# Optimization experiments

Hardware: AMD Instinct MI355X
Metric: run time of the kernel (lower is better)

## Reference

```python
import jax, jax.numpy as jnp
import numpy as np

B, N, C, H, NUM, K = 4, 4096, 256, 512, 4, 10
GS1 = H // NUM   # feature-group size = 128
GS2 = N // NUM   # point-group size  = 1024


def _mlp2(x, w1, b1, w2, b2):
    # Linear -> ReLU -> Linear
    return jax.nn.relu(x @ w1 + b1) @ w2 + b2


def setup_inputs() -> dict:
    key = jax.random.key(0)
    ks = jax.random.split(key, 32)
    s = 0.02
    def w(i, shape):
        return jax.random.normal(ks[i], shape, dtype=jnp.float32) * s
    return {
        "features": jax.random.normal(ks[0], (B, C, N), dtype=jnp.float32),
        "xyz": jax.random.uniform(ks[1], (B, N, 3), dtype=jnp.float32),
        # fc1 / fc2 (stored [in,out] for x @ W)
        "fc1_w": w(2, (C, H)), "fc1_b": jnp.zeros((H,), jnp.float32),
        "fc2_w": w(3, (H, C)), "fc2_b": jnp.zeros((C,), jnp.float32),
        # fc_delta: Linear(3,H) -> ReLU -> Linear(H,H)
        "fd1_w": w(4, (3, H)), "fd1_b": jnp.zeros((H,), jnp.float32),
        "fd2_w": w(5, (H, H)), "fd2_b": jnp.zeros((H,), jnp.float32),
        # fc_gamma: Linear(H,H) -> ReLU -> Linear(H,H)
        "fg1_w": w(6, (H, H)), "fg1_b": jnp.zeros((H,), jnp.float32),
        "fg2_w": w(7, (H, H)), "fg2_b": jnp.zeros((H,), jnp.float32),
        # fc_gamma_2: Linear(GS1,GS1) -> ReLU -> Linear(GS1,GS1)
        "fgh1_w": w(8, (GS1, GS1)), "fgh1_b": jnp.zeros((GS1,), jnp.float32),
        "fgh2_w": w(9, (GS1, GS1)), "fgh2_b": jnp.zeros((GS1,), jnp.float32),
        # projections (no bias)
        "wqs": w(10, (H, H)), "wks": w(11, (H, H)), "wvs": w(12, (H, H)),
        "wqs2": w(13, (GS1, GS1)), "wks2": w(14, (GS1, GS1)),
    }


def reference(features, xyz, fc1_w, fc1_b, fc2_w, fc2_b, fd1_w, fd1_b, fd2_w, fd2_b,
              fg1_w, fg1_b, fg2_w, fg2_b, fgh1_w, fgh1_b, fgh2_w, fgh2_b,
              wqs, wks, wvs, wqs2, wks2):
    pre = features                                  # [B, C, N]
    x = jnp.swapaxes(features, 1, 2) @ fc1_w + fc1_b  # [B, N, H]

    # ---- attn1: feature-group subtraction attention (shared small weights per group)
    xg = x.reshape(B, N, NUM, GS1)
    q1 = jnp.einsum('bngc,cd->bngd', xg, wqs2)
    k1 = jnp.einsum('bngc,cd->bngd', xg, wks2)
    a1 = _mlp2(q1 - k1, fgh1_w, fgh1_b, fgh2_w, fgh2_b)
    a1 = jax.nn.softmax(a1 / np.sqrt(GS1).astype(np.float32), axis=1)  # softmax over points
    attn1 = a1.reshape(B, N, H)

    # ---- attn2: point-group attention. NOTE: source loop reuses stale index `i`
    # (== NUM-1) so every group is computed from the LAST point group; we replicate that.
    gf2 = x[:, (NUM - 1) * GS2:NUM * GS2, :]        # [B, GS2, H]
    q2 = gf2 @ wqs
    k2 = gf2 @ wks
    a2 = _mlp2(q2 - k2, fg1_w, fg1_b, fg2_w, fg2_b)
    a2 = jax.nn.softmax(a2 / np.sqrt(H).astype(np.float32), axis=-2)
    attn2 = jnp.tile(a2, (1, NUM, 1))               # [B, N, H]

    attn = attn1 + attn2
    v = x @ wvs                                     # [B, N, H]

    # ---- KNN positional encoding
    # square_distance
    d = (jnp.sum(xyz ** 2, -1)[:, :, None] + jnp.sum(xyz ** 2, -1)[:, None, :]
         - 2.0 * jnp.einsum('bnd,bmd->bnm', xyz, xyz))  # [B, N, N]
    knn_idx = jax.lax.top_k(-d, K)[1]               # [B, N, K] smallest distances
    knn_xyz = jax.vmap(lambda pts, idx: pts[idx])(xyz, knn_idx)  # [B, N, K, 3]
    pos_enc = _mlp2(xyz[:, :, None, :] - knn_xyz, fd1_w, fd1_b, fd2_w, fd2_b)  # [B,N,K,H]
    pos_enc = pos_enc.mean(axis=2)                  # [B, N, H]

    res = attn * (v + pos_enc)                      # einsum('bmf,bmf->bmf')
    new_features = jnp.swapaxes(res @ fc2_w + fc2_b, 1, 2) + pre  # [B, C, N]
    return (new_features, xyz)
```

## Files before the change

kernel.cpp:

```cpp
#include <hip/hip_runtime.h>
#include <cstdio>

typedef long long ll;
typedef unsigned long long ull;
typedef unsigned short ushort_t;
typedef __bf16 bf16x8 __attribute__((ext_vector_type(8)));
typedef float f32x4 __attribute__((ext_vector_type(4)));
typedef float f32x2 __attribute__((ext_vector_type(2)));

#define BB 4
#define NN 4096
#define CC 256
#define HH 512
#define GNUM 4
#define GS1 128
#define KNN 10

#define SC1 0.08838834764831845f
#define SC2 0.044194173824159216f

__device__ inline unsigned pk2(float x, float y) {
  unsigned a = __float_as_uint(x), b = __float_as_uint(y);
  a = (a + 0x7FFFu + ((a >> 16) & 1u)) >> 16;
  b = (b + 0x7FFFu + ((b >> 16) & 1u)) >> 16;
  return a | (b << 16);
}
__device__ inline ushort_t bf1(float x) {
  unsigned a = __float_as_uint(x);
  return (ushort_t)((a + 0x7FFFu + ((a >> 16) & 1u)) >> 16);
}
__device__ inline float b2f(ushort_t u) { return __uint_as_float((unsigned)u << 16); }
__device__ inline int sw16(int r) { return ((r ^ (r >> 3)) & 7) << 4; }

__device__ inline void xcd_map(int& bx, int& by, int& bz) {
  const int nx = gridDim.x, ny = gridDim.y;
  const int nwg = nx * ny * gridDim.z;
  const int bidf = blockIdx.x + nx * (blockIdx.y + ny * blockIdx.z);
  const int lid = (bidf & 7) * (nwg >> 3) + (bidf >> 3);
  bx = lid % nx;
  const int rem = lid / nx;
  by = rem % ny;
  bz = rem / ny;
}

template<bool ATRANS, bool ABF, bool BSUB, int EPI>
__global__ __launch_bounds__(256, 2) void mgemm_k(
    const void* __restrict__ Ain, const float* __restrict__ Bw,
    const float* __restrict__ Bw2,
    const float* __restrict__ bias, void* __restrict__ CoutV,
    const float* __restrict__ pre,
    int M, int N, int K, int lda, ll strideA, ll strideC)
{
  int bx, by, z;
  xcd_map(bx, by, z);
  const int bm = by * 128;
  const int bn = bx * 128;
  __shared__ alignas(16) char smem[32768];
  char* smA = smem;
  char* smB = smem + 16384;
  const int tid = threadIdx.x;
  const int lane = tid & 63, w = tid >> 6;
  const int lr = lane & 15, lg = lane >> 4;
  const int wm = (w & 1) * 64, wn = (w >> 1) * 64;

  const ushort_t* Ab = ABF ? ((const ushort_t*)Ain + (ll)z * strideA) : nullptr;
  const float*    Af = ABF ? nullptr : ((const float*)Ain + (ll)z * strideA);

  f32x4 acc[4][4] = {};

  for (int k0 = 0; k0 < K; k0 += 64) {
    if (ABF) {
      #pragma unroll
      for (int p = 0; p < 4; ++p) {
        const int i = p * 256 + tid;
        const int r = i >> 3, c8 = (i & 7) * 8;
        const uint4 v = *reinterpret_cast<const uint4*>(Ab + (ll)(bm + r) * lda + (k0 + c8));
        *reinterpret_cast<uint4*>(smA + r * 128 + ((c8 * 2) ^ sw16(r))) = v;
      }
    } else if (ATRANS) {
      #pragma unroll
      for (int p = 0; p < 2; ++p) {
        const int bb = p * 256 + tid;
        const int mb = (bb & 31) * 4, kb = (bb >> 5) * 4;
        const float4 l0 = *reinterpret_cast<const float4*>(Af + (ll)(k0 + kb + 0) * lda + (bm + mb));
        const float4 l1 = *reinterpret_cast<const float4*>(Af + (ll)(k0 + kb + 1) * lda + (bm + mb));
        const float4 l2 = *reinterpret_cast<const float4*>(Af + (ll)(k0 + kb + 2) * lda + (bm + mb));
        const float4 l3 = *reinterpret_cast<const float4*>(Af + (ll)(k0 + kb + 3) * lda + (bm + mb));
        *reinterpret_cast<uint2*>(smA + (mb + 0) * 128 + ((kb * 2) ^ sw16(mb + 0))) = make_uint2(pk2(l0.x, l1.x), pk2(l2.x, l3.x));
        *reinterpret_cast<uint2*>(smA + (mb + 1) * 128 + ((kb * 2) ^ sw16(mb + 1))) = make_uint2(pk2(l0.y, l1.y), pk2(l2.y, l3.y));
        *reinterpret_cast<uint2*>(smA + (mb + 2) * 128 + ((kb * 2) ^ sw16(mb + 2))) = make_uint2(pk2(l0.z, l1.z), pk2(l2.z, l3.z));
        *reinterpret_cast<uint2*>(smA + (mb + 3) * 128 + ((kb * 2) ^ sw16(mb + 3))) = make_uint2(pk2(l0.w, l1.w), pk2(l2.w, l3.w));
      }
    }
    #pragma unroll
    for (int p = 0; p < 2; ++p) {
      const int bb = p * 256 + tid;
      const int nb = (bb & 31) * 4, kb = (bb >> 5) * 4;
      float4 l0 = *reinterpret_cast<const float4*>(Bw + (ll)(k0 + kb + 0) * N + (bn + nb));
      float4 l1 = *reinterpret_cast<const float4*>(Bw + (ll)(k0 + kb + 1) * N + (bn + nb));
      float4 l2 = *reinterpret_cast<const float4*>(Bw + (ll)(k0 + kb + 2) * N + (bn + nb));
      float4 l3 = *reinterpret_cast<const float4*>(Bw + (ll)(k0 + kb + 3) * N + (bn + nb));
      if (BSUB) {
        const float4 m0 = *reinterpret_cast<const float4*>(Bw2 + (ll)(k0 + kb + 0) * N + (bn + nb));
        const float4 m1 = *reinterpret_cast<const float4*>(Bw2 + (ll)(k0 + kb + 1) * N + (bn + nb));
        const float4 m2 = *reinterpret_cast<const float4*>(Bw2 + (ll)(k0 + kb + 2) * N + (bn + nb));
        const float4 m3 = *reinterpret_cast<const float4*>(Bw2 + (ll)(k0 + kb + 3) * N + (bn + nb));
        l0.x -= m0.x; l0.y -= m0.y; l0.z -= m0.z; l0.w -= m0.w;
        l1.x -= m1.x; l1.y -= m1.y; l1.z -= m1.z; l1.w -= m1.w;
        l2.x -= m2.x; l2.y -= m2.y; l2.z -= m2.z; l2.w -= m2.w;
        l3.x -= m3.x; l3.y -= m3.y; l3.z -= m3.z; l3.w -= m3.w;
      }
      *reinterpret_cast<uint2*>(smB + (nb + 0) * 128 + ((kb * 2) ^ sw16(nb + 0))) = make_uint2(pk2(l0.x, l1.x), pk2(l2.x, l3.x));
      *reinterpret_cast<uint2*>(smB + (nb + 1) * 128 + ((kb * 2) ^ sw16(nb + 1))) = make_uint2(pk2(l0.y, l1.y), pk2(l2.y, l3.y));
      *reinterpret_cast<uint2*>(smB + (nb + 2) * 128 + ((kb * 2) ^ sw16(nb + 2))) = make_uint2(pk2(l0.z, l1.z), pk2(l2.z, l3.z));
      *reinterpret_cast<uint2*>(smB + (nb + 3) * 128 + ((kb * 2) ^ sw16(nb + 3))) = make_uint2(pk2(l0.w, l1.w), pk2(l2.w, l3.w));
    }
    __syncthreads();

    #pragma unroll
    for (int ks = 0; ks < 2; ++ks) {
      bf16x8 af[4], bfr[4];
      #pragma unroll
      for (int mi = 0; mi < 4; ++mi) {
        const int r = wm + mi * 16 + lr;
        af[mi] = *reinterpret_cast<const bf16x8*>(smA + r * 128 + ((((ks << 2) + lg) << 4) ^ sw16(r)));
      }
      #pragma unroll
      for (int ni = 0; ni < 4; ++ni) {
        const int r = wn + ni * 16 + lr;
        bfr[ni] = *reinterpret_cast<const bf16x8*>(smB + r * 128 + ((((ks << 2) + lg) << 4) ^ sw16(r)));
      }
      #pragma unroll
      for (int mi = 0; mi < 4; ++mi)
        #pragma unroll
        for (int ni = 0; ni < 4; ++ni)
          acc[mi][ni] = __builtin_amdgcn_mfma_f32_16x16x32_bf16(af[mi], bfr[ni], acc[mi][ni], 0, 0, 0);
    }
    __syncthreads();
  }

  #pragma unroll
  for (int ni = 0; ni < 4; ++ni) {
    const int col = bn + wn + ni * 16 + lr;
    const float bv = (EPI != 0) ? bias[col] : 0.f;
    #pragma unroll
    for (int mi = 0; mi < 4; ++mi) {
      const int row0 = bm + wm + mi * 16 + lg * 4;
      if (EPI == 4) {
        float* Cout = (float*)CoutV;
        const size_t o = ((size_t)z * N + col) * (size_t)M + row0;
        const float4 pv = *reinterpret_cast<const float4*>(pre + o);
        float4 r;
        r.x = acc[mi][ni][0] + bv + pv.x;
        r.y = acc[mi][ni][1] + bv + pv.y;
        r.z = acc[mi][ni][2] + bv + pv.z;
        r.w = acc[mi][ni][3] + bv + pv.w;
        *reinterpret_cast<float4*>(Cout + o) = r;
      } else {
        ushort_t* Co = (ushort_t*)CoutV + (ll)z * strideC;
        #pragma unroll
        for (int i = 0; i < 4; ++i) {
          float val = acc[mi][ni][i] + bv;
          if (EPI == 2) val = fmaxf(val, 0.f);
          Co[(ll)(row0 + i) * N + col] = bf1(val);
        }
      }
    }
  }
}

__global__ __launch_bounds__(256, 2) void gemm_vpe_k(
    const ushort_t* __restrict__ X, const ushort_t* __restrict__ HM,
    const float* __restrict__ wv, const float* __restrict__ w2,
    const float* __restrict__ bias, ushort_t* __restrict__ Cout)
{
  int bx, by, z;
  xcd_map(bx, by, z);
  const int bm = by * 128;
  const int bn = bx * 128;
  __shared__ alignas(16) char smem[32768];
  char* smA = smem;
  char* smB = smem + 16384;
  const int tid = threadIdx.x;
  const int lane = tid & 63, w = tid >> 6;
  const int lr = lane & 15, lg = lane >> 4;
  const int wm = (w & 1) * 64, wn = (w >> 1) * 64;

  f32x4 acc[4][4] = {};

  for (int k0 = 0; k0 < 1024; k0 += 64) {
    const ushort_t* A = (k0 < 512) ? X : HM;
    const float* Bw = (k0 < 512) ? wv : w2;
    const int kk = k0 & 511;
    #pragma unroll
    for (int p = 0; p < 4; ++p) {
      const int i = p * 256 + tid;
      const int r = i >> 3, c8 = (i & 7) * 8;
      const uint4 v = *reinterpret_cast<const uint4*>(A + (ll)(bm + r) * 512 + (kk + c8));
      *reinterpret_cast<uint4*>(smA + r * 128 + ((c8 * 2) ^ sw16(r))) = v;
    }
    #pragma unroll
    for (int p = 0; p < 2; ++p) {
      const int bb = p * 256 + tid;
      const int nb = (bb & 31) * 4, kb = (bb >> 5) * 4;
      const float4 l0 = *reinterpret_cast<const float4*>(Bw + (ll)(kk + kb + 0) * 512 + (bn + nb));
      const float4 l1 = *reinterpret_cast<const float4*>(Bw + (ll)(kk + kb + 1) * 512 + (bn + nb));
      const float4 l2 = *reinterpret_cast<const float4*>(Bw + (ll)(kk + kb + 2) * 512 + (bn + nb));
      const float4 l3 = *reinterpret_cast<const float4*>(Bw + (ll)(kk + kb + 3) * 512 + (bn + nb));
      *reinterpret_cast<uint2*>(smB + (nb + 0) * 128 + ((kb * 2) ^ sw16(nb + 0))) = make_uint2(pk2(l0.x, l1.x), pk2(l2.x, l3.x));
      *reinterpret_cast<uint2*>(smB + (nb + 1) * 128 + ((kb * 2) ^ sw16(nb + 1))) = make_uint2(pk2(l0.y, l1.y), pk2(l2.y, l3.y));
      *reinterpret_cast<uint2*>(smB + (nb + 2) * 128 + ((kb * 2) ^ sw16(nb + 2))) = make_uint2(pk2(l0.z, l1.z), pk2(l2.z, l3.z));
      *reinterpret_cast<uint2*>(smB + (nb + 3) * 128 + ((kb * 2) ^ sw16(nb + 3))) = make_uint2(pk2(l0.w, l1.w), pk2(l2.w, l3.w));
    }
    __syncthreads();

    #pragma unroll
    for (int ks = 0; ks < 2; ++ks) {
      bf16x8 af[4], bfr[4];
      #pragma unroll
      for (int mi = 0; mi < 4; ++mi) {
        const int r = wm + mi * 16 + lr;
        af[mi] = *reinterpret_cast<const bf16x8*>(smA + r * 128 + ((((ks << 2) + lg) << 4) ^ sw16(r)));
      }
      #pragma unroll
      for (int ni = 0; ni < 4; ++ni) {
        const int r = wn + ni * 16 + lr;
        bfr[ni] = *reinterpret_cast<const bf16x8*>(smB + r * 128 + ((((ks << 2) + lg) << 4) ^ sw16(r)));
      }
      #pragma unroll
      for (int mi = 0; mi < 4; ++mi)
        #pragma unroll
        for (int ni = 0; ni < 4; ++ni)
          acc[mi][ni] = __builtin_amdgcn_mfma_f32_16x16x32_bf16(af[mi], bfr[ni], acc[mi][ni], 0, 0, 0);
    }
    __syncthreads();
  }

  #pragma unroll
  for (int ni = 0; ni < 4; ++ni) {
    const int col = bn + wn + ni * 16 + lr;
    const float bv = bias[col];
    #pragma unroll
    for (int mi = 0; mi < 4; ++mi) {
      const int row0 = bm + wm + mi * 16 + lg * 4;
      #pragma unroll
      for (int i = 0; i < 4; ++i)
        Cout[(ll)(row0 + i) * 512 + col] = bf1(acc[mi][ni][i] + bv);
    }
  }
}

__device__ __forceinline__ void gemm128(const char* smA, const char* smW, int wrow, int lr, int lg,
                                        f32x4 acc[8]) {
  #pragma unroll
  for (int ks = 0; ks < 4; ++ks) {
    const int koff = (ks * 4 + lg) * 16;
    const int ra = wrow + lr;
    const bf16x8 a = *reinterpret_cast<const bf16x8*>(smA + ra * 256 + (koff ^ sw16(ra)));
    #pragma unroll
    for (int ni = 0; ni < 8; ++ni) {
      const int rn = ni * 16 + lr;
      const bf16x8 b = *reinterpret_cast<const bf16x8*>(smW + rn * 256 + (koff ^ sw16(rn)));
      acc[ni] = __builtin_amdgcn_mfma_f32_16x16x32_bf16(a, b, acc[ni], 0, 0, 0);
    }
  }
}

__device__ __forceinline__ void stageWT(const float* __restrict__ W, char* smW, int tid) {
  #pragma unroll
  for (int p = 0; p < 2; ++p) {
    const int bb = p * 512 + tid;
    const int nb = (bb & 31) * 4, kb = (bb >> 5) * 4;
    const float4 l0 = *reinterpret_cast<const float4*>(W + (kb + 0) * 128 + nb);
    const float4 l1 = *reinterpret_cast<const float4*>(W + (kb + 1) * 128 + nb);
    const float4 l2 = *reinterpret_cast<const float4*>(W + (kb + 2) * 128 + nb);
    const float4 l3 = *reinterpret_cast<const float4*>(W + (kb + 3) * 128 + nb);
    *reinterpret_cast<uint2*>(smW + (nb + 0) * 256 + ((kb * 2) ^ sw16(nb + 0))) = make_uint2(pk2(l0.x, l1.x), pk2(l2.x, l3.x));
    *reinterpret_cast<uint2*>(smW + (nb + 1) * 256 + ((kb * 2) ^ sw16(nb + 1))) = make_uint2(pk2(l0.y, l1.y), pk2(l2.y, l3.y));
    *reinterpret_cast<uint2*>(smW + (nb + 2) * 256 + ((kb * 2) ^ sw16(nb + 2))) = make_uint2(pk2(l0.z, l1.z), pk2(l2.z, l3.z));
    *reinterpret_cast<uint2*>(smW + (nb + 3) * 256 + ((kb * 2) ^ sw16(nb + 3))) = make_uint2(pk2(l0.w, l1.w), pk2(l2.w, l3.w));
  }
}

__global__ __launch_bounds__(512, 4) void fused1_k(
    const ushort_t* __restrict__ X,
    const float* __restrict__ wqs2, const float* __restrict__ wks2,
    const float* __restrict__ w2g, const float* __restrict__ b2g,
    const float* __restrict__ w3g, const float* __restrict__ b3g,
    ushort_t* __restrict__ P)
{
  __shared__ alignas(16) char smT[32768];
  __shared__ alignas(16) char smW[32768];
  const int tid = threadIdx.x;
  const int lane = tid & 63, w = tid >> 6;
  const int lr = lane & 15, lg = lane >> 4;
  const int wrow = w * 16;
  const ll blockRow = (ll)blockIdx.x * 128;
  const ushort_t* Xb = X + blockRow * 128;

  float b2r[8], b3r[8];
  #pragma unroll
  for (int ni = 0; ni < 8; ++ni) { b2r[ni] = b2g[ni * 16 + lr]; b3r[ni] = b3g[ni * 16 + lr]; }

  #pragma unroll
  for (int p = 0; p < 4; ++p) {
    const int i = p * 512 + tid;
    const int r = i >> 4, c8 = (i & 15) * 8;
    const uint4 v = *reinterpret_cast<const uint4*>(Xb + (ll)r * 128 + c8);
    *reinterpret_cast<uint4*>(smT + r * 256 + ((c8 * 2) ^ sw16(r))) = v;
  }
  #pragma unroll
  for (int p = 0; p < 2; ++p) {
    const int bb = p * 512 + tid;
    const int nb = (bb & 31) * 4, kb = (bb >> 5) * 4;
    float4 l0 = *reinterpret_cast<const float4*>(wqs2 + (kb + 0) * 128 + nb);
    float4 l1 = *reinterpret_cast<const float4*>(wqs2 + (kb + 1) * 128 + nb);
    float4 l2 = *reinterpret_cast<const float4*>(wqs2 + (kb + 2) * 128 + nb);
    float4 l3 = *reinterpret_cast<const float4*>(wqs2 + (kb + 3) * 128 + nb);
    const float4 m0 = *reinterpret_cast<const float4*>(wks2 + (kb + 0) * 128 + nb);
    const float4 m1 = *reinterpret_cast<const float4*>(wks2 + (kb + 1) * 128 + nb);
    const float4 m2 = *reinterpret_cast<const float4*>(wks2 + (kb + 2) * 128 + nb);
    const float4 m3 = *reinterpret_cast<const float4*>(wks2 + (kb + 3) * 128 + nb);
    l0.x -= m0.x; l0.y -= m0.y; l0.z -= m0.z; l0.w -= m0.w;
    l1.x -= m1.x; l1.y -= m1.y; l1.z -= m1.z; l1.w -= m1.w;
    l2.x -= m2.x; l2.y -= m2.y; l2.z -= m2.z; l2.w -= m2.w;
    l3.x -= m3.x; l3.y -= m3.y; l3.z -= m3.z; l3.w -= m3.w;
    *reinterpret_cast<uint2*>(smW + (nb + 0) * 256 + ((kb * 2) ^ sw16(nb + 0))) = make_uint2(pk2(l0.x, l1.x), pk2(l2.x, l3.x));
    *reinterpret_cast<uint2*>(smW + (nb + 1) * 256 + ((kb * 2) ^ sw16(nb + 1))) = make_uint2(pk2(l0.y, l1.y), pk2(l2.y, l3.y));
    *reinterpret_cast<uint2*>(smW + (nb + 2) * 256 + ((kb * 2) ^ sw16(nb + 2))) = make_uint2(pk2(l0.z, l1.z), pk2(l2.z, l3.z));
    *reinterpret_cast<uint2*>(smW + (nb + 3) * 256 + ((kb * 2) ^ sw16(nb + 3))) = make_uint2(pk2(l0.w, l1.w), pk2(l2.w, l3.w));
  }
  __syncthreads();

  f32x4 acc[8];
  #pragma unroll
  for (int ni = 0; ni < 8; ++ni) acc[ni] = f32x4{0.f, 0.f, 0.f, 0.f};
  gemm128(smT, smW, wrow, lr, lg, acc);
  __syncthreads();

  #pragma unroll
  for (int ni = 0; ni < 8; ++ni)
    #pragma unroll
    for (int i = 0; i < 4; ++i) {
      const int r = wrow + lg * 4 + i;
      *reinterpret_cast<ushort_t*>(smT + r * 256 + (((ni * 16 + lr) * 2) ^ sw16(r))) = bf1(acc[ni][i]);
    }
  stageWT(w2g, smW, tid);
  __syncthreads();

  #pragma unroll
  for (int ni = 0; ni < 8; ++ni) acc[ni] = f32x4{0.f, 0.f, 0.f, 0.f};
  gemm128(smT, smW, wrow, lr, lg, acc);
  __syncthreads();

  #pragma unroll
  for (int ni = 0; ni < 8; ++ni)
    #pragma unroll
    for (int i = 0; i < 4; ++i) {
      const int r = wrow + lg * 4 + i;
      *reinterpret_cast<ushort_t*>(smT + r * 256 + (((ni * 16 + lr) * 2) ^ sw16(r))) =
          bf1(fmaxf(acc[ni][i] + b2r[ni], 0.f));
    }
  stageWT(w3g, smW, tid);
  __syncthreads();

  #pragma unroll
  for (int ni = 0; ni < 8; ++ni) acc[ni] = f32x4{0.f, 0.f, 0.f, 0.f};
  gemm128(smT, smW, wrow, lr, lg, acc);

  #pragma unroll
  for (int ni = 0; ni < 8; ++ni)
    #pragma unroll
    for (int i = 0; i < 4; ++i) {
      const ll r = blockRow + wrow + lg * 4 + i;
      P[r * 128 + ni * 16 + lr] = bf1(acc[ni][i] + b3r[ni]);
    }
}

__device__ inline void omax_upd(float& m, float& s, float v, float scale) {
  if (v > m) { s = s * expf((m - v) * scale) + 1.0f; m = v; }
  else       { s += expf((v - m) * scale); }
}
__device__ inline void omax_merge(float& m, float& s, float m2, float s2, float scale) {
  if (m2 > m) { s = s * expf((m - m2) * scale) + s2; m = m2; }
  else        { s += s2 * expf((m2 - m) * scale); }
}

__global__ __launch_bounds__(256) void red12_k(const ushort_t* __restrict__ P, const ushort_t* __restrict__ A2,
                                               float* __restrict__ PM1, float* __restrict__ PS1,
                                               float* __restrict__ PM2, float* __restrict__ PS2) {
  __shared__ float sm[256], ss[256];
  if (blockIdx.x < 512) {
    const int bid = blockIdx.x;
    const int b = bid >> 7, g = (bid >> 5) & 3, seg = bid & 31;
    const int d = threadIdx.x & 127, half = threadIdx.x >> 7;
    const size_t base = (size_t)b * NN * HH + g * GS1 + d;
    float m = -3.4e38f, s = 0.f;
    const int n0 = seg * 128 + half * 64;
    for (int n = n0; n < n0 + 64; ++n)
      omax_upd(m, s, b2f(P[base + (size_t)n * HH]), SC1);
    sm[threadIdx.x] = m; ss[threadIdx.x] = s;
    __syncthreads();
    if (half == 0) {
      omax_merge(m, s, sm[threadIdx.x + 128], ss[threadIdx.x + 128], SC1);
      const int c = b * HH + g * GS1 + d;
      PM1[(size_t)seg * 2048 + c] = m;
      PS1[(size_t)seg * 2048 + c] = s;
    }
  } else {
    const int bid = blockIdx.x - 512;
    const int b = bid >> 5, hb = (bid >> 3) & 3, seg = bid & 7;
    const int hl = threadIdx.x & 127, half = threadIdx.x >> 7;
    const int h = hb * 128 + hl;
    const size_t base = (size_t)b * 1024 * HH + h;
    float m = -3.4e38f, s = 0.f;
    const int r0 = seg * 128 + half * 64;
    for (int r = r0; r < r0 + 64; ++r)
      omax_upd(m, s, b2f(A2[base + (size_t)r * HH]), SC2);
    sm[threadIdx.x] = m; ss[threadIdx.x] = s;
    __syncthreads();
    if (half == 0) {
      omax_merge(m, s, sm[threadIdx.x + 128], ss[threadIdx.x + 128], SC2);
      const int c = b * HH + h;
      PM2[(size_t)seg * 2048 + c] = m;
      PS2[(size_t)seg * 2048 + c] = s;
    }
  }
}

__global__ __launch_bounds__(256) void combine12_k(const float* __restrict__ PM1, const float* __restrict__ PS1,
                                                   const float* __restrict__ PM2, const float* __restrict__ PS2,
                                                   float* __restrict__ M1, float* __restrict__ R1,
                                                   float* __restrict__ M2, float* __restrict__ R2) {
  if (blockIdx.x < 8) {
    const int c = blockIdx.x * 256 + threadIdx.x;
    float m = -3.4e38f, s = 0.f;
    for (int seg = 0; seg < 32; ++seg)
      omax_merge(m, s, PM1[(size_t)seg * 2048 + c], PS1[(size_t)seg * 2048 + c], SC1);
    M1[c] = m;
    R1[c] = 1.0f / s;
  } else {
    const int c = (blockIdx.x - 8) * 256 + threadIdx.x;
    float m = -3.4e38f, s = 0.f;
    for (int seg = 0; seg < 8; ++seg)
      omax_merge(m, s, PM2[(size_t)seg * 2048 + c], PS2[(size_t)seg * 2048 + c], SC2);
    M2[c] = m;
    R2[c] = 1.0f / s;
  }
}

__global__ __launch_bounds__(512, 4) void knn9_k(const float* __restrict__ xyz, int* __restrict__ idx) {
  const int blk = blockIdx.x;
  const int b = blk >> 7;
  const int q0 = (blk & 127) * 32;
  const float* xb = xyz + (size_t)b * NN * 3;
  const int tid = threadIdx.x;
  const int lane = tid & 63, w = tid >> 6;

  __shared__ alignas(16) float px[2048], py[2048], pz[2048], pw2[2048];
  __shared__ unsigned short candI[32][64];
  __shared__ int cnt[32];

  float qx[4], qy[4], qz[4], qn2[4];
  #pragma unroll
  for (int qq = 0; qq < 4; ++qq) {
    const int n = q0 + w * 4 + qq;
    qx[qq] = xb[n * 3]; qy[qq] = xb[n * 3 + 1]; qz[qq] = xb[n * 3 + 2];
    qn2[qq] = fmaf(qz[qq], qz[qq], fmaf(qy[qq], qy[qq], qx[qq] * qx[qq]));
  }
  if (tid < 32) cnt[tid] = 0;

  f32x2 mind[4];
  #pragma unroll
  for (int qq = 0; qq < 4; ++qq) mind[qq] = f32x2{3.4e38f, 3.4e38f};

  #pragma unroll
  for (int c = 0; c < 2; ++c) {
    __syncthreads();
    #pragma unroll
    for (int i = 0; i < 4; ++i) {
      const int p = i * 512 + tid;
      const int g = c * 2048 + p;
      const float x = xb[g * 3], y = xb[g * 3 + 1], z = xb[g * 3 + 2];
      px[p] = x; py[p] = y; pz[p] = z;
      pw2[p] = fmaf(z, z, fmaf(y, y, x * x));
    }
    __syncthreads();
    #pragma unroll 4
    for (int i = 0; i < 16; ++i) {
      const int p2 = i * 128 + lane * 2;
      const f32x2 x = *reinterpret_cast<const f32x2*>(&px[p2]);
      const f32x2 y = *reinterpret_cast<const f32x2*>(&py[p2]);
      const f32x2 z = *reinterpret_cast<const f32x2*>(&pz[p2]);
      const f32x2 pn = *reinterpret_cast<const f32x2*>(&pw2[p2]);
      #pragma unroll
      for (int qq = 0; qq < 4; ++qq) {
        f32x2 dot = x * qx[qq] + y * qy[qq] + z * qz[qq];
        const f32x2 dist = (pn + qn2[qq]) - (dot + dot);
        mind[qq].x = fminf(mind[qq].x, dist.x);
        mind[qq].y = fminf(mind[qq].y, dist.y);
      }
    }
  }

  float T[4];
  #pragma unroll
  for (int qq = 0; qq < 4; ++qq) {
    float v = fminf(mind[qq].x, mind[qq].y);
    #pragma unroll
    for (int k = 2; k <= 64; k <<= 1) {
      #pragma unroll
      for (int j = k >> 1; j > 0; j >>= 1) {
        const float o = __shfl_xor(v, j);
        const bool keepMin = (((lane & k) == 0) == ((lane & j) == 0));
        v = keepMin ? fminf(v, o) : fmaxf(v, o);
      }
    }
    T[qq] = __shfl(v, 9);
  }

  #pragma unroll
  for (int cc = 0; cc < 2; ++cc) {
    const int c = 1 - cc;
    if (c == 0) {
      __syncthreads();
      #pragma unroll
      for (int i = 0; i < 4; ++i) {
        const int p = i * 512 + tid;
        const float x = xb[p * 3], y = xb[p * 3 + 1], z = xb[p * 3 + 2];
        px[p] = x; py[p] = y; pz[p] = z;
        pw2[p] = fmaf(z, z, fmaf(y, y, x * x));
      }
      __syncthreads();
    }
    const int gbase = c * 2048;
    #pragma unroll 2
    for (int i = 0; i < 16; ++i) {
      const int p2 = i * 128 + lane * 2;
      const f32x2 x = *reinterpret_cast<const f32x2*>(&px[p2]);
      const f32x2 y = *reinterpret_cast<const f32x2*>(&py[p2]);
      const f32x2 z = *reinterpret_cast<const f32x2*>(&pz[p2]);
      const f32x2 pn = *reinterpret_cast<const f32x2*>(&pw2[p2]);
      #pragma unroll
      for (int qq = 0; qq < 4; ++qq) {
        f32x2 dot = x * qx[qq] + y * qy[qq] + z * qz[qq];
        const f32x2 dist = (pn + qn2[qq]) - (dot + dot);
        const int q = w * 4 + qq;
        if (dist.x <= T[qq]) {
          const int slot = atomicAdd(&cnt[q], 1);
          if (slot < 64) candI[q][slot] = (unsigned short)(gbase + p2);
        }
        if (dist.y <= T[qq]) {
          const int slot = atomicAdd(&cnt[q], 1);
          if (slot < 64) candI[q][slot] = (unsigned short)(gbase + p2 + 1);
        }
      }
    }
  }

  #pragma unroll
  for (int qq = 0; qq < 4; ++qq) {
    const int q = w * 4 + qq;
    const int cN = cnt[q] < 64 ? cnt[q] : 64;
    ull cv = ~0ull;
    if (lane < cN) {
      const int p = candI[q][lane];
      const float x = xb[p * 3], y = xb[p * 3 + 1], z = xb[p * 3 + 2];
      const float pn2 = fmaf(z, z, fmaf(y, y, x * x));
      const float dot = fmaf(qz[qq], z, fmaf(qy[qq], y, qx[qq] * x));
      const float dist = fmaf(-2.f, dot, qn2[qq] + pn2);
      const unsigned u = __float_as_uint(dist);
      const unsigned key = u ^ (unsigned)(((int)u >> 31) | 0x80000000);
      cv = ((ull)key << 12) | (unsigned)p;
    }
    #pragma unroll
    for (int k = 2; k <= 64; k <<= 1) {
      #pragma unroll
      for (int j = k >> 1; j > 0; j >>= 1) {
        const ull o = __shfl_xor(cv, j);
        const bool keepMin = (((lane & k) == 0) == ((lane & j) == 0));
        const bool oLess = o < cv;
        cv = (keepMin == oLess) ? o : cv;
      }
    }
    if (lane < KNN) idx[((size_t)(b * NN + q0 + q)) * KNN + lane] = (int)(cv & 0xFFFull);
  }
}

__global__ __launch_bounds__(256) void posenc_k(const float* __restrict__ xyz, const int* __restrict__ idx,
                                                const float* __restrict__ fd1w, const float* __restrict__ fd1b,
                                                ushort_t* __restrict__ hmean, float* __restrict__ outxyz) {
  const int bn = blockIdx.x;
  const int b = bn >> 12, n = bn & (NN - 1);
  const float* xb = xyz + (size_t)b * NN * 3;
  const float qx = xb[n * 3], qy = xb[n * 3 + 1], qz = xb[n * 3 + 2];
  __shared__ float dxyz[KNN][3];
  if (threadIdx.x < KNN) {
    const int m = idx[(size_t)bn * KNN + threadIdx.x];
    dxyz[threadIdx.x][0] = qx - xb[m * 3];
    dxyz[threadIdx.x][1] = qy - xb[m * 3 + 1];
    dxyz[threadIdx.x][2] = qz - xb[m * 3 + 2];
  }
  if (threadIdx.x >= 64 && threadIdx.x < 67) {
    const int c = threadIdx.x - 64;
    outxyz[(size_t)bn * 3 + c] = xb[n * 3 + c];
  }
  __syncthreads();
  for (int h = threadIdx.x; h < HH; h += 256) {
    const float w0 = fd1w[h], w1 = fd1w[HH + h], w2 = fd1w[2 * HH + h], bb = fd1b[h];
    float acc = 0.f;
    #pragma unroll
    for (int k = 0; k < KNN; ++k)
      acc += fmaxf(fmaf(dxyz[k][2], w2, fmaf(dxyz[k][1], w1, dxyz[k][0] * w0)) + bb, 0.f);
    hmean[(size_t)bn * HH + h] = bf1(acc * 0.1f);
  }
}

__global__ __launch_bounds__(256) void res_k(const ushort_t* __restrict__ P, const ushort_t* __restrict__ A2,
                                             const ushort_t* __restrict__ V,
                                             const float* __restrict__ M1, const float* __restrict__ R1,
                                             const float* __restrict__ M2, const float* __restrict__ R2,
                                             ushort_t* __restrict__ R) {
  const size_t i8 = (size_t)blockIdx.x * 256 + threadIdx.x;
  const size_t i = i8 * 8;
  const int b = (int)(i >> 21);
  const int n = (int)((i >> 9) & (NN - 1));
  const int h = (int)(i & (HH - 1));
  const int c = (b << 9) + h;
  const size_t j = (((size_t)b * 1024 + (n & 1023)) << 9) + h;
  const uint4 pu = *reinterpret_cast<const uint4*>(P + i);
  const uint4 au = *reinterpret_cast<const uint4*>(A2 + j);
  const uint4 vu = *reinterpret_cast<const uint4*>(V + i);
  float m1[8], r1[8], m2[8], r2[8];
  *reinterpret_cast<float4*>(m1) = *reinterpret_cast<const float4*>(M1 + c);
  *reinterpret_cast<float4*>(m1 + 4) = *reinterpret_cast<const float4*>(M1 + c + 4);
  *reinterpret_cast<float4*>(r1) = *reinterpret_cast<const float4*>(R1 + c);
  *reinterpret_cast<float4*>(r1 + 4) = *reinterpret_cast<const float4*>(R1 + c + 4);
  *reinterpret_cast<float4*>(m2) = *reinterpret_cast<const float4*>(M2 + c);
  *reinterpret_cast<float4*>(m2 + 4) = *reinterpret_cast<const float4*>(M2 + c + 4);
  *reinterpret_cast<float4*>(r2) = *reinterpret_cast<const float4*>(R2 + c);
  *reinterpret_cast<float4*>(r2 + 4) = *reinterpret_cast<const float4*>(R2 + c + 4);
  const unsigned* pw = reinterpret_cast<const unsigned*>(&pu);
  const unsigned* aw = reinterpret_cast<const unsigned*>(&au);
  const unsigned* vw = reinterpret_cast<const unsigned*>(&vu);
  float r[8];
  #pragma unroll
  for (int e = 0; e < 8; ++e) {
    const unsigned wsel = (e >> 1);
    const ushort_t pv = (ushort_t)((pw[wsel] >> ((e & 1) * 16)) & 0xFFFF);
    const ushort_t av = (ushort_t)((aw[wsel] >> ((e & 1) * 16)) & 0xFFFF);
    const ushort_t vv = (ushort_t)((vw[wsel] >> ((e & 1) * 16)) & 0xFFFF);
    r[e] = (expf((b2f(pv) - m1[e]) * SC1) * r1[e] + expf((b2f(av) - m2[e]) * SC2) * r2[e]) * b2f(vv);
  }
  uint4 ru;
  ru.x = pk2(r[0], r[1]);
  ru.y = pk2(r[2], r[3]);
  ru.z = pk2(r[4], r[5]);
  ru.w = pk2(r[6], r[7]);
  *reinterpret_cast<uint4*>(R + i) = ru;
}

extern "C" void kernel_launch(void* const* d_in, const int* in_sizes, int n_in,
                              void* d_out, int out_size, void* d_ws, size_t ws_size,
                              hipStream_t stream) {
  const float* features = (const float*)d_in[0];
  const float* xyz      = (const float*)d_in[1];
  const float* fc1_w    = (const float*)d_in[2];
  const float* fc1_b    = (const float*)d_in[3];
  const float* fc2_w    = (const float*)d_in[4];
  const float* fc2_b    = (const float*)d_in[5];
  const float* fd1_w    = (const float*)d_in[6];
  const float* fd1_b    = (const float*)d_in[7];
  const float* fd2_w    = (const float*)d_in[8];
  const float* fd2_b    = (const float*)d_in[9];
  const float* fg1_w    = (const float*)d_in[10];
  const float* fg1_b    = (const float*)d_in[11];
  const float* fg2_w    = (const float*)d_in[12];
  const float* fg2_b    = (const float*)d_in[13];
  const float* fgh1_w   = (const float*)d_in[14];
  const float* fgh1_b   = (const float*)d_in[15];
  const float* fgh2_w   = (const float*)d_in[16];
  const float* fgh2_b   = (const float*)d_in[17];
  const float* wqs      = (const float*)d_in[18];
  const float* wks      = (const float*)d_in[19];
  const float* wvs      = (const float*)d_in[20];
  const float* wqs2     = (const float*)d_in[21];
  const float* wks2     = (const float*)d_in[22];
  float* out = (float*)d_out;

  const size_t BNH = (size_t)BB * NN * HH;
  float* PM1 = (float*)d_ws;
  float* PS1 = PM1 + 32 * 2048;
  float* PM2 = PS1 + 32 * 2048;
  float* PS2 = PM2 + 8 * 2048;
  float* M1  = PS2 + 8 * 2048;
  float* R1  = M1 + 2048;
  float* M2  = R1 + 2048;
  float* R2  = M2 + 2048;
  int*   IDX = (int*)(R2 + 2048);
  ushort_t* Xh = (ushort_t*)(IDX + (size_t)BB * NN * KNN);
  ushort_t* P  = Xh + BNH;
  ushort_t* HM = P + BNH;
  ushort_t* V  = HM + BNH;
  ushort_t* R  = V + BNH;
  ushort_t* S1 = R + BNH;
  ushort_t* S2 = S1 + (size_t)BB * 1024 * HH;
  const size_t need = ((char*)(S2 + (size_t)BB * 1024 * HH)) - (char*)d_ws;
  if (ws_size < need) {
    fprintf(stderr, "kernel_launch: ws too small: %zu < %zu\n", ws_size, need);
    return;
  }

  mgemm_k<true, false, false, 1><<<dim3(HH / 128, NN / 128, BB), 256, 0, stream>>>(
      features, fc1_w, nullptr, fc1_b, Xh, nullptr, NN, HH, CC, NN, (ll)CC * NN, (ll)NN * HH);

  fused1_k<<<512, 512, 0, stream>>>(Xh, wqs2, wks2, fgh1_w, fgh1_b, fgh2_w, fgh2_b, P);

  mgemm_k<false, true, true, 0><<<dim3(HH / 128, 1024 / 128, BB), 256, 0, stream>>>(
      Xh + (size_t)3072 * HH, wqs, wks, nullptr, S1, nullptr, 1024, HH, HH, HH, (ll)NN * HH, (ll)1024 * HH);
  mgemm_k<false, true, false, 2><<<dim3(HH / 128, BB * 1024 / 128, 1), 256, 0, stream>>>(
      S1, fg1_w, nullptr, fg1_b, S2, nullptr, BB * 1024, HH, HH, HH, 0, 0);
  mgemm_k<false, true, false, 1><<<dim3(HH / 128, BB * 1024 / 128, 1), 256, 0, stream>>>(
      S2, fg2_w, nullptr, fg2_b, S1, nullptr, BB * 1024, HH, HH, HH, 0, 0);

  red12_k<<<640, 256, 0, stream>>>(P, S1, PM1, PS1, PM2, PS2);
  combine12_k<<<16, 256, 0, stream>>>(PM1, PS1, PM2, PS2, M1, R1, M2, R2);

  knn9_k<<<BB * NN / 32, 512, 0, stream>>>(xyz, IDX);
  posenc_k<<<BB * NN, 256, 0, stream>>>(xyz, IDX, fd1_w, fd1_b, HM, out + (size_t)BB * CC * NN);

  gemm_vpe_k<<<dim3(HH / 128, BB * NN / 128, 1), 256, 0, stream>>>(
      Xh, HM, wvs, fd2_w, fd2_b, V);

  res_k<<<(int)(BNH / 8 / 256), 256, 0, stream>>>(P, S1, V, M1, R1, M2, R2, R);

  mgemm_k<false, true, false, 4><<<dim3(CC / 128, NN / 128, BB), 256, 0, stream>>>(
      R, fc2_w, nullptr, fc2_b, out, features, NN, CC, HH, HH, (ll)NN * HH, 0);
}
```

Before: 256.3 us.

## Pre-convert weights to transposed bf16 once and halve KNN queries per block

Adds a weight-conversion kernel that writes every GEMM weight matrix once per call as transposed bf16, with wqs-wks and wqs2-wks2 pre-subtracted. All GEMM kernels and fused1_k then stage B tiles with plain 16-byte bf16 loads instead of per-tile fp32 loads, subtraction, and packing repeated across every block. Separately, the KNN kernel handles 16 queries per block instead of 32, doubling the grid for more parallelism, with a higher occupancy hint. The cost is one extra launch and about 3 MB of weight traffic, while the KNN blocks each restage the full point cloud in shared memory, now twice as often.

```diff
diff --git a/kernel.cpp b/kernel.cpp
--- a/kernel.cpp
+++ b/kernel.cpp
@@ -18,6 +18,18 @@
 
 #define SC1 0.08838834764831845f
 #define SC2 0.044194173824159216f
+
+#define OFF_FC1T   0
+#define OFF_WD2T   131072
+#define OFF_FGH1T  147456
+#define OFF_FGH2T  163840
+#define OFF_WDT    180224
+#define OFF_FG1T   442368
+#define OFF_FG2T   704512
+#define OFF_WVST   966656
+#define OFF_FD2T   1228800
+#define OFF_FC2T   1490944
+#define WT_TOTAL   1622016
 
 __device__ inline unsigned pk2(float x, float y) {
   unsigned a = __float_as_uint(x), b = __float_as_uint(y);
@@ -43,10 +55,44 @@
   bz = rem / ny;
 }
 
-template<bool ATRANS, bool ABF, bool BSUB, int EPI>
+__global__ __launch_bounds__(256) void wconv_k(
+    const float* __restrict__ fc1w, const float* __restrict__ wqs2, const float* __restrict__ wks2,
+    const float* __restrict__ fgh1, const float* __restrict__ fgh2,
+    const float* __restrict__ wqs, const float* __restrict__ wks,
+    const float* __restrict__ fg1, const float* __restrict__ fg2,
+    const float* __restrict__ wvs, const float* __restrict__ fd2,
+    const float* __restrict__ fc2w, ushort_t* __restrict__ WT)
+{
+  const int gc = blockIdx.x * 256 + threadIdx.x;
+  const int e0 = gc * 8;
+  if (e0 >= WT_TOTAL) return;
+  const float* src = nullptr; const float* src2 = nullptr;
+  int off, Kd, Nd;
+  if (e0 < OFF_WD2T)        { src = fc1w;             off = OFF_FC1T;  Kd = 256; Nd = 512; }
+  else if (e0 < OFF_FGH1T)  { src = wqs2; src2 = wks2; off = OFF_WD2T;  Kd = 128; Nd = 128; }
+  else if (e0 < OFF_FGH2T)  { src = fgh1;             off = OFF_FGH1T; Kd = 128; Nd = 128; }
+  else if (e0 < OFF_WDT)    { src = fgh2;             off = OFF_FGH2T; Kd = 128; Nd = 128; }
+  else if (e0 < OFF_FG1T)   { src = wqs;  src2 = wks;  off = OFF_WDT;   Kd = 512; Nd = 512; }
+  else if (e0 < OFF_FG2T)   { src = fg1;              off = OFF_FG1T;  Kd = 512; Nd = 512; }
+  else if (e0 < OFF_WVST)   { src = fg2;              off = OFF_FG2T;  Kd = 512; Nd = 512; }
+  else if (e0 < OFF_FD2T)   { src = wvs;              off = OFF_WVST;  Kd = 512; Nd = 512; }
+  else if (e0 < OFF_FC2T)   { src = fd2;              off = OFF_FD2T;  Kd = 512; Nd = 512; }
+  else                      { src = fc2w;             off = OFF_FC2T;  Kd = 512; Nd = 256; }
+  const int local = e0 - off;
+  const int n = local / Kd, k0 = local % Kd;
+  ushort_t outv[8];
+  #pragma unroll
+  for (int j = 0; j < 8; ++j) {
+    float v = src[(ll)(k0 + j) * Nd + n];
+    if (src2) v -= src2[(ll)(k0 + j) * Nd + n];
+    outv[j] = bf1(v);
+  }
+  *reinterpret_cast<uint4*>(WT + e0) = *reinterpret_cast<uint4*>(outv);
+}
+
+template<bool ATRANS, int EPI>
 __global__ __launch_bounds__(256, 2) void mgemm_k(
-    const void* __restrict__ Ain, const float* __restrict__ Bw,
-    const float* __restrict__ Bw2,
+    const void* __restrict__ Ain, const ushort_t* __restrict__ BT,
     const float* __restrict__ bias, void* __restrict__ CoutV,
     const float* __restrict__ pre,
     int M, int N, int K, int lda, ll strideA, ll strideC)
@@ -63,13 +109,13 @@
   const int lr = lane & 15, lg = lane >> 4;
   const int wm = (w & 1) * 64, wn = (w >> 1) * 64;
 
-  const ushort_t* Ab = ABF ? ((const ushort_t*)Ain + (ll)z * strideA) : nullptr;
-  const float*    Af = ABF ? nullptr : ((const float*)Ain + (ll)z * strideA);
+  const ushort_t* Ab = ATRANS ? nullptr : ((const ushort_t*)Ain + (ll)z * strideA);
+  const float*    Af = ATRANS ? ((const float*)Ain + (ll)z * strideA) : nullptr;
 
   f32x4 acc[4][4] = {};
 
   for (int k0 = 0; k0 < K; k0 += 64) {
-    if (ABF) {
+    if (!ATRANS) {
       #pragma unroll
       for (int p = 0; p < 4; ++p) {
         const int i = p * 256 + tid;
@@ -77,7 +123,7 @@
         const uint4 v = *reinterpret_cast<const uint4*>(Ab + (ll)(bm + r) * lda + (k0 + c8));
         *reinterpret_cast<uint4*>(smA + r * 128 + ((c8 * 2) ^ sw16(r))) = v;
       }
-    } else if (ATRANS) {
+    } else {
       #pragma unroll
       for (int p = 0; p < 2; ++p) {
         const int bb = p * 256 + tid;
@@ -93,27 +139,11 @@
       }
     }
     #pragma unroll
-    for (int p = 0; p < 2; ++p) {
-      const int bb = p * 256 + tid;
-      const int nb = (bb & 31) * 4, kb = (bb >> 5) * 4;
-      float4 l0 = *reinterpret_cast<const float4*>(Bw + (ll)(k0 + kb + 0) * N + (bn + nb));
-      float4 l1 = *reinterpret_cast<const float4*>(Bw + (ll)(k0 + kb + 1) * N + (bn + nb));
-      float4 l2 = *reinterpret_cast<const float4*>(Bw + (ll)(k0 + kb + 2) * N + (bn + nb));
-      float4 l3 = *reinterpret_cast<const float4*>(Bw + (ll)(k0 + kb + 3) * N + (bn + nb));
-      if (BSUB) {
-        const float4 m0 = *reinterpret_cast<const float4*>(Bw2 + (ll)(k0 + kb + 0) * N + (bn + nb));
-        const float4 m1 = *reinterpret_cast<const float4*>(Bw2 + (ll)(k0 + kb + 1) * N + (bn + nb));
-        const float4 m2 = *reinterpret_cast<const float4*>(Bw2 + (ll)(k0 + kb + 2) * N + (bn + nb));
-        const float4 m3 = *reinterpret_cast<const float4*>(Bw2 + (ll)(k0 + kb + 3) * N + (bn + nb));
-        l0.x -= m0.x; l0.y -= m0.y; l0.z -= m0.z; l0.w -= m0.w;
-        l1.x -= m1.x; l1.y -= m1.y; l1.z -= m1.z; l1.w -= m1.w;
-        l2.x -= m2.x; l2.y -= m2.y; l2.z -= m2.z; l2.w -= m2.w;
-        l3.x -= m3.x; l3.y -= m3.y; l3.z -= m3.z; l3.w -= m3.w;
-      }
-      *reinterpret_cast<uint2*>(smB + (nb + 0) * 128 + ((kb * 2) ^ sw16(nb + 0))) = make_uint2(pk2(l0.x, l1.x), pk2(l2.x, l3.x));
-      *reinterpret_cast<uint2*>(smB + (nb + 1) * 128 + ((kb * 2) ^ sw16(nb + 1))) = make_uint2(pk2(l0.y, l1.y), pk2(l2.y, l3.y));
-      *reinterpret_cast<uint2*>(smB + (nb + 2) * 128 + ((kb * 2) ^ sw16(nb + 2))) = make_uint2(pk2(l0.z, l1.z), pk2(l2.z, l3.z));
-      *reinterpret_cast<uint2*>(smB + (nb + 3) * 128 + ((kb * 2) ^ sw16(nb + 3))) = make_uint2(pk2(l0.w, l1.w), pk2(l2.w, l3.w));
+    for (int p = 0; p < 4; ++p) {
+      const int i = p * 256 + tid;
+      const int r = i >> 3, c8 = (i & 7) * 8;
+      const uint4 v = *reinterpret_cast<const uint4*>(BT + (ll)(bn + r) * K + (k0 + c8));
+      *reinterpret_cast<uint4*>(smB + r * 128 + ((c8 * 2) ^ sw16(r))) = v;
     }
     __syncthreads();
 
@@ -171,7 +201,7 @@
 
 __global__ __launch_bounds__(256, 2) void gemm_vpe_k(
     const ushort_t* __restrict__ X, const ushort_t* __restrict__ HM,
-    const float* __restrict__ wv, const float* __restrict__ w2,
+    const ushort_t* __restrict__ wvT, const ushort_t* __restrict__ w2T,
     const float* __restrict__ bias, ushort_t* __restrict__ Cout)
 {
   int bx, by, z;
@@ -190,7 +220,7 @@
 
   for (int k0 = 0; k0 < 1024; k0 += 64) {
     const ushort_t* A = (k0 < 512) ? X : HM;
-    const float* Bw = (k0 < 512) ? wv : w2;
+    const ushort_t* BT = (k0 < 512) ? wvT : w2T;
     const int kk = k0 & 511;
     #pragma unroll
     for (int p = 0; p < 4; ++p) {
@@ -200,17 +230,11 @@
       *reinterpret_cast<uint4*>(smA + r * 128 + ((c8 * 2) ^ sw16(r))) = v;
     }
     #pragma unroll
-    for (int p = 0; p < 2; ++p) {
-      const int bb = p * 256 + tid;
-      const int nb = (bb & 31) * 4, kb = (bb >> 5) * 4;
-      const float4 l0 = *reinterpret_cast<const float4*>(Bw + (ll)(kk + kb + 0) * 512 + (bn + nb));
-      const float4 l1 = *reinterpret_cast<const float4*>(Bw + (ll)(kk + kb + 1) * 512 + (bn + nb));
-      const float4 l2 = *reinterpret_cast<const float4*>(Bw + (ll)(kk + kb + 2) * 512 + (bn + nb));
-      const float4 l3 = *reinterpret_cast<const float4*>(Bw + (ll)(kk + kb + 3) * 512 + (bn + nb));
-      *reinterpret_cast<uint2*>(smB + (nb + 0) * 128 + ((kb * 2) ^ sw16(nb + 0))) = make_uint2(pk2(l0.x, l1.x), pk2(l2.x, l3.x));
-      *reinterpret_cast<uint2*>(smB + (nb + 1) * 128 + ((kb * 2) ^ sw16(nb + 1))) = make_uint2(pk2(l0.y, l1.y), pk2(l2.y, l3.y));
-      *reinterpret_cast<uint2*>(smB + (nb + 2) * 128 + ((kb * 2) ^ sw16(nb + 2))) = make_uint2(pk2(l0.z, l1.z), pk2(l2.z, l3.z));
-      *reinterpret_cast<uint2*>(smB + (nb + 3) * 128 + ((kb * 2) ^ sw16(nb + 3))) = make_uint2(pk2(l0.w, l1.w), pk2(l2.w, l3.w));
+    for (int p = 0; p < 4; ++p) {
+      const int i = p * 256 + tid;
+      const int r = i >> 3, c8 = (i & 7) * 8;
+      const uint4 v = *reinterpret_cast<const uint4*>(BT + (ll)(bn + r) * 512 + (kk + c8));
+      *reinterpret_cast<uint4*>(smB + r * 128 + ((c8 * 2) ^ sw16(r))) = v;
     }
     __syncthreads();
 
@@ -266,27 +290,21 @@
   }
 }
 
-__device__ __forceinline__ void stageWT(const float* __restrict__ W, char* smW, int tid) {
-  #pragma unroll
-  for (int p = 0; p < 2; ++p) {
-    const int bb = p * 512 + tid;
-    const int nb = (bb & 31) * 4, kb = (bb >> 5) * 4;
-    const float4 l0 = *reinterpret_cast<const float4*>(W + (kb + 0) * 128 + nb);
-    const float4 l1 = *reinterpret_cast<const float4*>(W + (kb + 1) * 128 + nb);
-    const float4 l2 = *reinterpret_cast<const float4*>(W + (kb + 2) * 128 + nb);
-    const float4 l3 = *reinterpret_cast<const float4*>(W + (kb + 3) * 128 + nb);
-    *reinterpret_cast<uint2*>(smW + (nb + 0) * 256 + ((kb * 2) ^ sw16(nb + 0))) = make_uint2(pk2(l0.x, l1.x), pk2(l2.x, l3.x));
-    *reinterpret_cast<uint2*>(smW + (nb + 1) * 256 + ((kb * 2) ^ sw16(nb + 1))) = make_uint2(pk2(l0.y, l1.y), pk2(l2.y, l3.y));
-    *reinterpret_cast<uint2*>(smW + (nb + 2) * 256 + ((kb * 2) ^ sw16(nb + 2))) = make_uint2(pk2(l0.z, l1.z), pk2(l2.z, l3.z));
-    *reinterpret_cast<uint2*>(smW + (nb + 3) * 256 + ((kb * 2) ^ sw16(nb + 3))) = make_uint2(pk2(l0.w, l1.w), pk2(l2.w, l3.w));
+__device__ __forceinline__ void stageWTb(const ushort_t* __restrict__ W, char* smW, int tid) {
+  #pragma unroll
+  for (int p = 0; p < 4; ++p) {
+    const int i = p * 512 + tid;
+    const int r = i >> 4, c8 = (i & 15) * 8;
+    const uint4 v = *reinterpret_cast<const uint4*>(W + r * 128 + c8);
+    *reinterpret_cast<uint4*>(smW + r * 256 + ((c8 * 2) ^ sw16(r))) = v;
   }
 }
 
 __global__ __launch_bounds__(512, 4) void fused1_k(
     const ushort_t* __restrict__ X,
-    const float* __restrict__ wqs2, const float* __restrict__ wks2,
-    const float* __restrict__ w2g, const float* __restrict__ b2g,
-    const float* __restrict__ w3g, const float* __restrict__ b3g,
+    const ushort_t* __restrict__ wd2T,
+    const ushort_t* __restrict__ w2T, const float* __restrict__ b2g,
+    const ushort_t* __restrict__ w3T, const float* __restrict__ b3g,
     ushort_t* __restrict__ P)
 {
   __shared__ alignas(16) char smT[32768];
@@ -309,27 +327,7 @@
     const uint4 v = *reinterpret_cast<const uint4*>(Xb + (ll)r * 128 + c8);
     *reinterpret_cast<uint4*>(smT + r * 256 + ((c8 * 2) ^ sw16(r))) = v;
   }
-  #pragma unroll
-  for (int p = 0; p < 2; ++p) {
-    const int bb = p * 512 + tid;
-    const int nb = (bb & 31) * 4, kb = (bb >> 5) * 4;
-    float4 l0 = *reinterpret_cast<const float4*>(wqs2 + (kb + 0) * 128 + nb);
-    float4 l1 = *reinterpret_cast<const float4*>(wqs2 + (kb + 1) * 128 + nb);
-    float4 l2 = *reinterpret_cast<const float4*>(wqs2 + (kb + 2) * 128 + nb);
-    float4 l3 = *reinterpret_cast<const float4*>(wqs2 + (kb + 3) * 128 + nb);
-    const float4 m0 = *reinterpret_cast<const float4*>(wks2 + (kb + 0) * 128 + nb);
-    const float4 m1 = *reinterpret_cast<const float4*>(wks2 + (kb + 1) * 128 + nb);
-    const float4 m2 = *reinterpret_cast<const float4*>(wks2 + (kb + 2) * 128 + nb);
-    const float4 m3 = *reinterpret_cast<const float4*>(wks2 + (kb + 3) * 128 + nb);
-    l0.x -= m0.x; l0.y -= m0.y; l0.z -= m0.z; l0.w -= m0.w;
-    l1.x -= m1.x; l1.y -= m1.y; l1.z -= m1.z; l1.w -= m1.w;
-    l2.x -= m2.x; l2.y -= m2.y; l2.z -= m2.z; l2.w -= m2.w;
-    l3.x -= m3.x; l3.y -= m3.y; l3.z -= m3.z; l3.w -= m3.w;
-    *reinterpret_cast<uint2*>(smW + (nb + 0) * 256 + ((kb * 2) ^ sw16(nb + 0))) = make_uint2(pk2(l0.x, l1.x), pk2(l2.x, l3.x));
-    *reinterpret_cast<uint2*>(smW + (nb + 1) * 256 + ((kb * 2) ^ sw16(nb + 1))) = make_uint2(pk2(l0.y, l1.y), pk2(l2.y, l3.y));
-    *reinterpret_cast<uint2*>(smW + (nb + 2) * 256 + ((kb * 2) ^ sw16(nb + 2))) = make_uint2(pk2(l0.z, l1.z), pk2(l2.z, l3.z));
-    *reinterpret_cast<uint2*>(smW + (nb + 3) * 256 + ((kb * 2) ^ sw16(nb + 3))) = make_uint2(pk2(l0.w, l1.w), pk2(l2.w, l3.w));
-  }
+  stageWTb(wd2T, smW, tid);
   __syncthreads();
 
   f32x4 acc[8];
@@ -345,7 +343,7 @@
       const int r = wrow + lg * 4 + i;
       *reinterpret_cast<ushort_t*>(smT + r * 256 + (((ni * 16 + lr) * 2) ^ sw16(r))) = bf1(acc[ni][i]);
     }
-  stageWT(w2g, smW, tid);
+  stageWTb(w2T, smW, tid);
   __syncthreads();
 
   #pragma unroll
@@ -361,7 +359,7 @@
       *reinterpret_cast<ushort_t*>(smT + r * 256 + (((ni * 16 + lr) * 2) ^ sw16(r))) =
           bf1(fmaxf(acc[ni][i] + b2r[ni], 0.f));
     }
-  stageWT(w3g, smW, tid);
+  stageWTb(w3T, smW, tid);
   __syncthreads();
 
   #pragma unroll
@@ -449,30 +447,30 @@
   }
 }
 
-__global__ __launch_bounds__(512, 4) void knn9_k(const float* __restrict__ xyz, int* __restrict__ idx) {
+__global__ __launch_bounds__(512, 8) void knn10_k(const float* __restrict__ xyz, int* __restrict__ idx) {
   const int blk = blockIdx.x;
-  const int b = blk >> 7;
-  const int q0 = (blk & 127) * 32;
+  const int b = blk >> 8;
+  const int q0 = (blk & 255) * 16;
   const float* xb = xyz + (size_t)b * NN * 3;
   const int tid = threadIdx.x;
   const int lane = tid & 63, w = tid >> 6;
 
   __shared__ alignas(16) float px[2048], py[2048], pz[2048], pw2[2048];
-  __shared__ unsigned short candI[32][64];
-  __shared__ int cnt[32];
-
-  float qx[4], qy[4], qz[4], qn2[4];
-  #pragma unroll
-  for (int qq = 0; qq < 4; ++qq) {
-    const int n = q0 + w * 4 + qq;
+  __shared__ unsigned short candI[16][64];
+  __shared__ int cnt[16];
+
+  float qx[2], qy[2], qz[2], qn2[2];
+  #pragma unroll
+  for (int qq = 0; qq < 2; ++qq) {
+    const int n = q0 + w * 2 + qq;
     qx[qq] = xb[n * 3]; qy[qq] = xb[n * 3 + 1]; qz[qq] = xb[n * 3 + 2];
     qn2[qq] = fmaf(qz[qq], qz[qq], fmaf(qy[qq], qy[qq], qx[qq] * qx[qq]));
   }
-  if (tid < 32) cnt[tid] = 0;
-
-  f32x2 mind[4];
-  #pragma unroll
-  for (int qq = 0; qq < 4; ++qq) mind[qq] = f32x2{3.4e38f, 3.4e38f};
+  if (tid < 16) cnt[tid] = 0;
+
+  f32x2 mind[2];
+  #pragma unroll
+  for (int qq = 0; qq < 2; ++qq) mind[qq] = f32x2{3.4e38f, 3.4e38f};
 
   #pragma unroll
   for (int c = 0; c < 2; ++c) {
@@ -494,7 +492,7 @@
       const f32x2 z = *reinterpret_cast<const f32x2*>(&pz[p2]);
       const f32x2 pn = *reinterpret_cast<const f32x2*>(&pw2[p2]);
       #pragma unroll
-      for (int qq = 0; qq < 4; ++qq) {
+      for (int qq = 0; qq < 2; ++qq) {
         f32x2 dot = x * qx[qq] + y * qy[qq] + z * qz[qq];
         const f32x2 dist = (pn + qn2[qq]) - (dot + dot);
         mind[qq].x = fminf(mind[qq].x, dist.x);
@@ -503,9 +501,9 @@
     }
   }
 
-  float T[4];
-  #pragma unroll
-  for (int qq = 0; qq < 4; ++qq) {
+  float T[2];
+  #pragma unroll
+  for (int qq = 0; qq < 2; ++qq) {
     float v = fminf(mind[qq].x, mind[qq].y);
     #pragma unroll
     for (int k = 2; k <= 64; k <<= 1) {
@@ -542,10 +540,10 @@
       const f32x2 z = *reinterpret_cast<const f32x2*>(&pz[p2]);
       const f32x2 pn = *reinterpret_cast<const f32x2*>(&pw2[p2]);
       #pragma unroll
-      for (int qq = 0; qq < 4; ++qq) {
+      for (int qq = 0; qq < 2; ++qq) {
         f32x2 dot = x * qx[qq] + y * qy[qq] + z * qz[qq];
         const f32x2 dist = (pn + qn2[qq]) - (dot + dot);
-        const int q = w * 4 + qq;
+        const int q = w * 2 + qq;
         if (dist.x <= T[qq]) {
           const int slot = atomicAdd(&cnt[q], 1);
           if (slot < 64) candI[q][slot] = (unsigned short)(gbase + p2);
@@ -559,8 +557,8 @@
   }
 
   #pragma unroll
-  for (int qq = 0; qq < 4; ++qq) {
-    const int q = w * 4 + qq;
+  for (int qq = 0; qq < 2; ++qq) {
+    const int q = w * 2 + qq;
     const int cN = cnt[q] < 64 ? cnt[q] : 64;
     ull cv = ~0ull;
     if (lane < cN) {
@@ -698,7 +696,8 @@
   float* M2  = R1 + 2048;
   float* R2  = M2 + 2048;
   int*   IDX = (int*)(R2 + 2048);
-  ushort_t* Xh = (ushort_t*)(IDX + (size_t)BB * NN * KNN);
+  ushort_t* WT = (ushort_t*)(IDX + (size_t)BB * NN * KNN);
+  ushort_t* Xh = WT + WT_TOTAL;
   ushort_t* P  = Xh + BNH;
   ushort_t* HM = P + BNH;
   ushort_t* V  = HM + BNH;
@@ -711,29 +710,32 @@
     return;
   }
 
-  mgemm_k<true, false, false, 1><<<dim3(HH / 128, NN / 128, BB), 256, 0, stream>>>(
-      features, fc1_w, nullptr, fc1_b, Xh, nullptr, NN, HH, CC, NN, (ll)CC * NN, (ll)NN * HH);
-
-  fused1_k<<<512, 512, 0, stream>>>(Xh, wqs2, wks2, fgh1_w, fgh1_b, fgh2_w, fgh2_b, P);
-
-  mgemm_k<false, true, true, 0><<<dim3(HH / 128, 1024 / 128, BB), 256, 0, stream>>>(
-      Xh + (size_t)3072 * HH, wqs, wks, nullptr, S1, nullptr, 1024, HH, HH, HH, (ll)NN * HH, (ll)1024 * HH);
-  mgemm_k<false, true, false, 2><<<dim3(HH / 128, BB * 1024 / 128, 1), 256, 0, stream>>>(
-      S1, fg1_w, nullptr, fg1_b, S2, nullptr, BB * 1024, HH, HH, HH, 0, 0);
-  mgemm_k<false, true, false, 1><<<dim3(HH / 128, BB * 1024 / 128, 1), 256, 0, stream>>>(
-      S2, fg2_w, nullptr, fg2_b, S1, nullptr, BB * 1024, HH, HH, HH, 0, 0);
+  wconv_k<<<(WT_TOTAL / 8 + 255) / 256, 256, 0, stream>>>(
+      fc1_w, wqs2, wks2, fgh1_w, fgh2_w, wqs, wks, fg1_w, fg2_w, wvs, fd2_w, fc2_w, WT);
+
+  mgemm_k<true, 1><<<dim3(HH / 128, NN / 128, BB), 256, 0, stream>>>(
+      features, WT + OFF_FC1T, fc1_b, Xh, nullptr, NN, HH, CC, NN, (ll)CC * NN, (ll)NN * HH);
+
+  fused1_k<<<512, 512, 0, stream>>>(Xh, WT + OFF_WD2T, WT + OFF_FGH1T, fgh1_b, WT + OFF_FGH2T, fgh2_b, P);
+
+  mgemm_k<false, 0><<<dim3(HH / 128, 1024 / 128, BB), 256, 0, stream>>>(
+      Xh + (size_t)3072 * HH, WT + OFF_WDT, nullptr, S1, nullptr, 1024, HH, HH, HH, (ll)NN * HH, (ll)1024 * HH);
+  mgemm_k<false, 2><<<dim3(HH / 128, BB * 1024 / 128, 1), 256, 0, stream>>>(
+      S1, WT + OFF_FG1T, fg1_b, S2, nullptr, BB * 1024, HH, HH, HH, 0, 0);
+  mgemm_k<false, 1><<<dim3(HH / 128, BB * 1024 / 128, 1), 256, 0, stream>>>(
+      S2, WT + OFF_FG2T, fg2_b, S1, nullptr, BB * 1024, HH, HH, HH, 0, 0);
 
   red12_k<<<640, 256, 0, stream>>>(P, S1, PM1, PS1, PM2, PS2);
   combine12_k<<<16, 256, 0, stream>>>(PM1, PS1, PM2, PS2, M1, R1, M2, R2);
 
-  knn9_k<<<BB * NN / 32, 512, 0, stream>>>(xyz, IDX);
+  knn10_k<<<BB * NN / 16, 512, 0, stream>>>(xyz, IDX);
   posenc_k<<<BB * NN, 256, 0, stream>>>(xyz, IDX, fd1_w, fd1_b, HM, out + (size_t)BB * CC * NN);
 
   gemm_vpe_k<<<dim3(HH / 128, BB * NN / 128, 1), 256, 0, stream>>>(
-      Xh, HM, wvs, fd2_w, fd2_b, V);
+      Xh, HM, WT + OFF_WVST, WT + OFF_FD2T, fd2_b, V);
 
   res_k<<<(int)(BNH / 8 / 256), 256, 0, stream>>>(P, S1, V, M1, R1, M2, R2, R);
 
-  mgemm_k<false, true, false, 4><<<dim3(CC / 128, NN / 128, BB), 256, 0, stream>>>(
-      R, fc2_w, nullptr, fc2_b, out, features, NN, CC, HH, HH, (ll)NN * HH, 0);
-}
+  mgemm_k<false, 4><<<dim3(CC / 128, NN / 128, BB), 256, 0, stream>>>(
+      R, WT + OFF_FC2T, fc2_b, out, features, NN, CC, HH, HH, (ll)NN * HH, 0);
+}
```

After: 235.3 us. -8.2%, faster.
